# Performance work log

Hardware: AMD Instinct MI355X
Metric: run time of the kernel (lower is better)

The kernel has to match this reference:

```python
import jax, jax.numpy as jnp
import numpy as np

B, C_MAX, T = 128, 272, 512
D1 = 320
NUM_SUBJECTS = 8
NUM_CHANNELS = [272, 256, 240, 224, 208, 270, 260, 248]


def setup_inputs() -> dict:
    key = jax.random.key(0)
    k_x, k_w, k_s = jax.random.split(key, 3)
    X = jax.random.normal(k_x, (B, C_MAX, T), dtype=jnp.float32)
    subject_idxs = jax.random.randint(k_s, (B,), 0, NUM_SUBJECTS)
    # Per-subject Conv1d(kernel=1, bias=False) weights, padded to C_MAX.
    # Original module only reads the first num_channels[s] input channels;
    # zeroing the padded columns reproduces that exactly.
    W = jax.random.normal(k_w, (NUM_SUBJECTS, D1, C_MAX), dtype=jnp.float32) * 0.02
    mask = np.zeros((NUM_SUBJECTS, 1, C_MAX), dtype=np.float32)
    for s, nc in enumerate(NUM_CHANNELS):
        mask[s, 0, :nc] = 1.0
    W = W * jnp.asarray(mask)
    return {"X": X, "subject_idxs": subject_idxs, "W": W}


def reference(X, subject_idxs, W):
    # Gather per-sample weight matrix [B, D1, C_MAX] by subject id, then
    # batched 1x1 conv == matmul over channels at every time step.
    Wsel = W[subject_idxs]                      # [B, D1, C]
    out = jnp.einsum("bdc,bct->bdt", Wsel, X)   # [B, D1, T]
    return out
```

## Files before the change

### kernel.cpp

```cpp
#include <hip/hip_runtime.h>

#define BB    128
#define CC    272
#define CPAD  288
#define TT    512
#define DD1   320
#define NT    64
#define MT    160
#define LDC   66

typedef float  f32x4  __attribute__((ext_vector_type(4)));
typedef __bf16 bf16x4 __attribute__((ext_vector_type(4)));
typedef __bf16 bf16x8 __attribute__((ext_vector_type(8)));

#define BAR() asm volatile("s_waitcnt lgkmcnt(0)\ns_barrier" ::: "memory")

__global__ __launch_bounds__(256)
void w_cvt(const float* __restrict__ W, __bf16* __restrict__ Wb) {
    const int i = blockIdx.x * 256 + threadIdx.x;
    const float4* src = (const float4*)W;
    const float4 a = src[2 * i];
    const float4 b = src[2 * i + 1];
    bf16x8 h = {(__bf16)a.x, (__bf16)a.y, (__bf16)a.z, (__bf16)a.w,
                (__bf16)b.x, (__bf16)b.y, (__bf16)b.z, (__bf16)b.w};
    *(bf16x8*)(Wb + 8 * i) = h;
}

template <bool WB16>
__global__ __launch_bounds__(256, 3)
void subj_conv_deep(const float*  __restrict__ X,
                    const int*    __restrict__ sidx,
                    const float*  __restrict__ W,
                    const __bf16* __restrict__ Wbf,
                    float*        __restrict__ out) {
    const int b  = blockIdx.x;
    const int T0 = blockIdx.y * NT;
    const int d0 = blockIdx.z * MT;
    const int s  = sidx[b];

    __shared__ __align__(16) __bf16 Xs[CPAD * LDC];

    const int tid  = threadIdx.x;
    const int lane = tid & 63;
    const int wv   = tid >> 6;
    const int wm   = wv & 1;
    const int wn   = wv >> 1;
    const int quad = lane >> 4;
    const int l16  = lane & 15;

    {
        const float* Xb = X + (size_t)b * CC * TT + T0;
        const int xr = tid >> 4;
        const int xt = (tid & 15) * 4;
#pragma unroll
        for (int pb = 0; pb < 3; ++pb) {
            float4 v[6];
#pragma unroll
            for (int q = 0; q < 6; ++q) {
                const int c = xr + 16 * (pb * 6 + q);
                v[q] = make_float4(0.f, 0.f, 0.f, 0.f);
                if (c < CC) v[q] = *(const float4*)(Xb + (size_t)c * TT + xt);
            }
#pragma unroll
            for (int q = 0; q < 6; ++q) {
                const int c = xr + 16 * (pb * 6 + q);
                bf16x4 h = {(__bf16)v[q].x, (__bf16)v[q].y,
                            (__bf16)v[q].z, (__bf16)v[q].w};
                *(bf16x4*)&Xs[c * LDC + xt] = h;
            }
        }
    }

    const size_t wrow = ((size_t)s * DD1 + d0 + wm * 80 + l16) * CC + quad * 8;
    const __bf16* Wp16 = Wbf + (WB16 ? wrow : 0);
    const float*  Wp32 = W   + (WB16 ? 0 : wrow);

    auto load_af = [&](int mt, int kc) -> bf16x8 {
        const int off = mt * 16 * CC + kc * 32;
        if constexpr (WB16) {
            return *(const bf16x8*)(Wp16 + off);
        } else {
            const float4 u0 = *(const float4*)(Wp32 + off);
            const float4 u1 = *(const float4*)(Wp32 + off + 4);
            return bf16x8{(__bf16)u0.x, (__bf16)u0.y, (__bf16)u0.z, (__bf16)u0.w,
                          (__bf16)u1.x, (__bf16)u1.y, (__bf16)u1.z, (__bf16)u1.w};
        }
    };

    bf16x8 af[2][5];
    bf16x8 bf[2][2];

#pragma unroll
    for (int mt = 0; mt < 5; ++mt) af[0][mt] = load_af(mt, 0);
#pragma unroll
    for (int mt = 0; mt < 5; ++mt) af[1][mt] = load_af(mt, 1);
    BAR();

    const int tc0 = wn * 32 + l16;
    const int tc1 = tc0 + 16;
#pragma unroll
    for (int j = 0; j < 8; ++j) {
        const int crow = (quad * 8 + j) * LDC;
        bf[0][0][j] = Xs[crow + tc0];
        bf[0][1][j] = Xs[crow + tc1];
    }

    f32x4 acc[5][2];
#pragma unroll
    for (int mt = 0; mt < 5; ++mt) {
        acc[mt][0] = (f32x4){0.f, 0.f, 0.f, 0.f};
        acc[mt][1] = (f32x4){0.f, 0.f, 0.f, 0.f};
    }

#pragma unroll
    for (int kc = 0; kc < 9; ++kc) {
        const int cur = kc & 1;
        const int nx  = cur ^ 1;
        if (kc + 1 < 9) {
#pragma unroll
            for (int j = 0; j < 8; ++j) {
                const int crow = ((kc + 1) * 32 + quad * 8 + j) * LDC;
                bf[nx][0][j] = Xs[crow + tc0];
                bf[nx][1][j] = Xs[crow + tc1];
            }
        }
#pragma unroll
        for (int mt = 0; mt < 5; ++mt) {
            acc[mt][0] = __builtin_amdgcn_mfma_f32_16x16x32_bf16(af[cur][mt], bf[cur][0],
                                                                 acc[mt][0], 0, 0, 0);
            acc[mt][1] = __builtin_amdgcn_mfma_f32_16x16x32_bf16(af[cur][mt], bf[cur][1],
                                                                 acc[mt][1], 0, 0, 0);
            if (kc + 2 < 8) {
                af[cur][mt] = load_af(mt, kc + 2);
            } else if (kc + 2 == 8) {
                bf16x8 a = {(__bf16)0.f, (__bf16)0.f, (__bf16)0.f, (__bf16)0.f,
                            (__bf16)0.f, (__bf16)0.f, (__bf16)0.f, (__bf16)0.f};
                if (quad < 2) a = load_af(mt, 8);
                af[cur][mt] = a;
            }
        }
    }

#pragma unroll
    for (int mt = 0; mt < 5; ++mt) {
        const int d = d0 + wm * 80 + mt * 16 + quad * 4;
#pragma unroll
        for (int nt = 0; nt < 2; ++nt) {
            float* ob = out + ((size_t)b * DD1 + d) * TT + T0 + wn * 32 + nt * 16 + l16;
#pragma unroll
            for (int r = 0; r < 4; ++r)
                ob[(size_t)r * TT] = acc[mt][nt][r];
        }
    }
}

extern "C" void kernel_launch(void* const* d_in, const int* in_sizes, int n_in,
                              void* d_out, int out_size, void* d_ws, size_t ws_size,
                              hipStream_t stream) {
    const float* X    = (const float*)d_in[0];
    const int*   sidx = (const int*)  d_in[1];
    const float* W    = (const float*)d_in[2];
    float*       out  = (float*)d_out;

    dim3 grid(BB, TT / NT, 2);
    dim3 block(256);

    const size_t need = (size_t)8 * DD1 * CC * sizeof(__bf16);
    if (d_ws && ws_size >= need) {
        __bf16* Wb = (__bf16*)d_ws;
        w_cvt<<<dim3(340), dim3(256), 0, stream>>>(W, Wb);
        subj_conv_deep<true><<<grid, block, 0, stream>>>(X, sidx, W, Wb, out);
    } else {
        subj_conv_deep<false><<<grid, block, 0, stream>>>(X, sidx, W, nullptr, out);
    }
}
```

Baseline: 167.1 us.

## Halve time tile to 32 columns and raise occupancy to four blocks per CU

Shrinks the per-block time tile from 64 to 32. This halves the LDS footprint and per-wave accumulators so four blocks can reside per CU instead of three. Each wave now issues one MFMA per weight fragment instead of two. This aims to hide memory latency through more thread-level parallelism, but doubles the number of blocks that each re-stream the same weight slice, lowering weight reuse.

New measurement: 188.3 us. 12.7% more time.

```diff
diff --git a/kernel.cpp b/kernel.cpp
--- a/kernel.cpp
+++ b/kernel.cpp
@@ -5,9 +5,9 @@
 #define CPAD  288
 #define TT    512
 #define DD1   320
-#define NT    64
+#define NT    32
 #define MT    160
-#define LDC   66
+#define LDC2  34
 
 typedef float  f32x4  __attribute__((ext_vector_type(4)));
 typedef __bf16 bf16x4 __attribute__((ext_vector_type(4)));
@@ -27,18 +27,18 @@
 }
 
 template <bool WB16>
-__global__ __launch_bounds__(256, 3)
-void subj_conv_deep(const float*  __restrict__ X,
-                    const int*    __restrict__ sidx,
-                    const float*  __restrict__ W,
-                    const __bf16* __restrict__ Wbf,
-                    float*        __restrict__ out) {
+__global__ __launch_bounds__(256, 4)
+void subj_conv_tlp(const float*  __restrict__ X,
+                   const int*    __restrict__ sidx,
+                   const float*  __restrict__ W,
+                   const __bf16* __restrict__ Wbf,
+                   float*        __restrict__ out) {
     const int b  = blockIdx.x;
     const int T0 = blockIdx.y * NT;
     const int d0 = blockIdx.z * MT;
     const int s  = sidx[b];
 
-    __shared__ __align__(16) __bf16 Xs[CPAD * LDC];
+    __shared__ __align__(16) __bf16 Xs[CPAD * LDC2];
 
     const int tid  = threadIdx.x;
     const int lane = tid & 63;
@@ -50,24 +50,21 @@
 
     {
         const float* Xb = X + (size_t)b * CC * TT + T0;
-        const int xr = tid >> 4;
-        const int xt = (tid & 15) * 4;
+        const int xr = tid >> 3;
+        const int xt = (tid & 7) * 4;
+        float4 v[9];
 #pragma unroll
-        for (int pb = 0; pb < 3; ++pb) {
-            float4 v[6];
+        for (int p = 0; p < 9; ++p) {
+            const int c = xr + 32 * p;
+            v[p] = make_float4(0.f, 0.f, 0.f, 0.f);
+            if (c < CC) v[p] = *(const float4*)(Xb + (size_t)c * TT + xt);
+        }
 #pragma unroll
-            for (int q = 0; q < 6; ++q) {
-                const int c = xr + 16 * (pb * 6 + q);
-                v[q] = make_float4(0.f, 0.f, 0.f, 0.f);
-                if (c < CC) v[q] = *(const float4*)(Xb + (size_t)c * TT + xt);
-            }
-#pragma unroll
-            for (int q = 0; q < 6; ++q) {
-                const int c = xr + 16 * (pb * 6 + q);
-                bf16x4 h = {(__bf16)v[q].x, (__bf16)v[q].y,
-                            (__bf16)v[q].z, (__bf16)v[q].w};
-                *(bf16x4*)&Xs[c * LDC + xt] = h;
-            }
+        for (int p = 0; p < 9; ++p) {
+            const int c = xr + 32 * p;
+            bf16x4 h = {(__bf16)v[p].x, (__bf16)v[p].y,
+                        (__bf16)v[p].z, (__bf16)v[p].w};
+            *(bf16x4*)&Xs[c * LDC2 + xt] = h;
         }
     }
 
@@ -88,7 +85,7 @@
     };
 
     bf16x8 af[2][5];
-    bf16x8 bf[2][2];
+    bf16x8 bfr[2];
 
 #pragma unroll
     for (int mt = 0; mt < 5; ++mt) af[0][mt] = load_af(mt, 0);
@@ -96,21 +93,15 @@
     for (int mt = 0; mt < 5; ++mt) af[1][mt] = load_af(mt, 1);
     BAR();
 
-    const int tc0 = wn * 32 + l16;
-    const int tc1 = tc0 + 16;
+    const int tc = wn * 16 + l16;
 #pragma unroll
-    for (int j = 0; j < 8; ++j) {
-        const int crow = (quad * 8 + j) * LDC;
-        bf[0][0][j] = Xs[crow + tc0];
-        bf[0][1][j] = Xs[crow + tc1];
-    }
+    for (int j = 0; j < 8; ++j)
+        bfr[0][j] = Xs[(quad * 8 + j) * LDC2 + tc];
 
-    f32x4 acc[5][2];
+    f32x4 acc[5];
 #pragma unroll
-    for (int mt = 0; mt < 5; ++mt) {
-        acc[mt][0] = (f32x4){0.f, 0.f, 0.f, 0.f};
-        acc[mt][1] = (f32x4){0.f, 0.f, 0.f, 0.f};
-    }
+    for (int mt = 0; mt < 5; ++mt)
+        acc[mt] = (f32x4){0.f, 0.f, 0.f, 0.f};
 
 #pragma unroll
     for (int kc = 0; kc < 9; ++kc) {
@@ -118,18 +109,13 @@
         const int nx  = cur ^ 1;
         if (kc + 1 < 9) {
 #pragma unroll
-            for (int j = 0; j < 8; ++j) {
-                const int crow = ((kc + 1) * 32 + quad * 8 + j) * LDC;
-                bf[nx][0][j] = Xs[crow + tc0];
-                bf[nx][1][j] = Xs[crow + tc1];
-            }
+            for (int j = 0; j < 8; ++j)
+                bfr[nx][j] = Xs[((kc + 1) * 32 + quad * 8 + j) * LDC2 + tc];
         }
 #pragma unroll
         for (int mt = 0; mt < 5; ++mt) {
-            acc[mt][0] = __builtin_amdgcn_mfma_f32_16x16x32_bf16(af[cur][mt], bf[cur][0],
-                                                                 acc[mt][0], 0, 0, 0);
-            acc[mt][1] = __builtin_amdgcn_mfma_f32_16x16x32_bf16(af[cur][mt], bf[cur][1],
-                                                                 acc[mt][1], 0, 0, 0);
+            acc[mt] = __builtin_amdgcn_mfma_f32_16x16x32_bf16(af[cur][mt], bfr[cur],
+                                                              acc[mt], 0, 0, 0);
             if (kc + 2 < 8) {
                 af[cur][mt] = load_af(mt, kc + 2);
             } else if (kc + 2 == 8) {
@@ -144,13 +130,10 @@
 #pragma unroll
     for (int mt = 0; mt < 5; ++mt) {
         const int d = d0 + wm * 80 + mt * 16 + quad * 4;
+        float* ob = out + ((size_t)b * DD1 + d) * TT + T0 + tc;
 #pragma unroll
-        for (int nt = 0; nt < 2; ++nt) {
-            float* ob = out + ((size_t)b * DD1 + d) * TT + T0 + wn * 32 + nt * 16 + l16;
-#pragma unroll
-            for (int r = 0; r < 4; ++r)
-                ob[(size_t)r * TT] = acc[mt][nt][r];
-        }
+        for (int r = 0; r < 4; ++r)
+            ob[(size_t)r * TT] = acc[mt][r];
     }
 }
 
@@ -169,8 +152,8 @@
     if (d_ws && ws_size >= need) {
         __bf16* Wb = (__bf16*)d_ws;
         w_cvt<<<dim3(340), dim3(256), 0, stream>>>(W, Wb);
-        subj_conv_deep<true><<<grid, block, 0, stream>>>(X, sidx, W, Wb, out);
+        subj_conv_tlp<true><<<grid, block, 0, stream>>>(X, sidx, W, Wb, out);
     } else {
-        subj_conv_deep<false><<<grid, block, 0, stream>>>(X, sidx, W, nullptr, out);
+        subj_conv_tlp<false><<<grid, block, 0, stream>>>(X, sidx, W, nullptr, out);
     }
 }
```
